# Optimization experiments

Hardware: AMD Instinct MI355X
Metric: run time of the kernel (lower is better)

Reference implementation:

```python
import jax, jax.numpy as jnp
import numpy as np

# Static dims (see shape_source)
B, S, D = 4, 4096, 1024      # batch, seq, d_model
H, E, K = 4096, 8, 2         # ffn hidden, num experts, top_k
GS = 128                     # group size = sqrt(B*S)
G = (B * S) // GS            # 128 groups, zero padding
CAP = 32                     # expert capacity after clamping


def setup_inputs() -> dict:
    key = jax.random.key(0)
    ks = jax.random.split(key, 8)
    std = jnp.float32(0.02)
    return {
        "x": jax.random.normal(ks[0], (B, S, D), jnp.float32),
        "gate_w": jax.random.normal(ks[1], (D, E), jnp.float32) * std,
        "gate_b": jnp.zeros((E,), jnp.float32),
        "keys": jax.random.normal(ks[2], (D, E, H), jnp.float32) * std,
        "key_b": jnp.zeros((E, H), jnp.float32),
        "values": jax.random.normal(ks[3], (H, E, D), jnp.float32) * std,
        "value_b": jnp.zeros((E, D), jnp.float32),
        "s_keys": jax.random.normal(ks[4], (D, 1, H), jnp.float32) * std,
        "s_key_b": jnp.zeros((1, H), jnp.float32),
        "s_values": jax.random.normal(ks[5], (H, 1, D), jnp.float32) * std,
        "s_value_b": jnp.zeros((1, D), jnp.float32),
    }


def reference(x, gate_w, gate_b, keys, key_b, values, value_b,
              s_keys, s_key_b, s_values, s_value_b):
    # ---- group tokens: [B,S,D] -> [G,GS,D] (B*S divisible by GS, no pad) ----
    xg = x.reshape(G, GS, D)

    # ---- Router (inference path: no aux loss) ----
    logits = jnp.einsum('gsd,de->gse', xg, gate_w) + gate_b          # [G,GS,E]
    probs = jax.nn.softmax(logits, axis=-1)
    gate, idx = jax.lax.top_k(probs, K)                              # [G,GS,K]
    mask = jax.nn.one_hot(idx, E, dtype=gate.dtype)                  # [G,GS,K,E]
    # position within each expert's capacity buffer (1-based where assigned)
    pos = jnp.cumsum(mask, axis=1) * mask                            # [G,GS,K,E]
    valid = (pos < CAP).astype(gate.dtype)
    pos_oh = jax.nn.one_hot(pos.astype(jnp.int32), CAP, dtype=gate.dtype)  # [G,GS,K,E,CAP]
    # combine tensor: sum over top-k, drop slot 0 (unassigned) -> [G,GS,E,CAP-1]
    combine = jnp.einsum('gsk,gske,gskec->gsec', gate, valid, pos_oh)[..., 1:]
    dispatch = (combine > 0).astype(x.dtype)                         # dispatch mask

    # ---- dispatch -> per-expert FFN -> combine ----
    exp_in = jnp.einsum('gsec,gsd->gecd', dispatch, xg)              # [G,E,CAP-1,D]
    h = jax.nn.gelu(jnp.einsum('gecd,deh->gech', exp_in, keys)
                    + key_b[None, :, None, :])                       # [G,E,CAP-1,H]
    eo = jnp.einsum('gech,hed->gecd', h, values) + value_b[None, :, None, :]
    moe = jnp.einsum('gsec,gecd->gsd', combine, eo)                  # [G,GS,D]

    # ---- shared expert (num_shared_experts == 1; mean over 1 is identity) ----
    sh = jax.nn.gelu(jnp.einsum('gsd,dh->gsh', xg, s_keys[:, 0, :]) + s_key_b[0])
    shared = jnp.einsum('gsh,hd->gsd', sh, s_values[:, 0, :]) + s_value_b[0]

    return (moe + shared).reshape(B, S, D)
```

## Files before the change

### kernel.cpp

```cpp
#include <hip/hip_runtime.h>
#include <hip/hip_bf16.h>

typedef unsigned short u16;
typedef __attribute__((ext_vector_type(8))) __bf16 bf16x8;
typedef __attribute__((ext_vector_type(4))) float f32x4;

#define TOK 16384
#define DM  1024
#define HD  4096
#define NE  8
#define NG  128
#define GSZ 128
#define CAPM 31
#define MEP (NG*32)

static __device__ __forceinline__ u16 f2b(float f) {
  union { float f; unsigned u; } v; v.f = f;
  unsigned r = v.u + 0x7fffu + ((v.u >> 16) & 1u);
  return (u16)(r >> 16);
}
static __device__ __forceinline__ float b2f(u16 u) {
  union { unsigned u; float f; } v; v.u = (unsigned)u << 16; return v.f;
}

static __device__ __forceinline__ float gelu_f(float x) {
  float y = 0.7978845608028654f * (x + 0.044715f * x * x * x);
  float t = __expf(-2.0f * fabsf(y));
  float th = (1.0f - t) / (1.0f + t);
  th = (y < 0.0f) ? -th : th;
  return 0.5f * x * (1.0f + th);
}

static __device__ __forceinline__ void gl2lds16(const void* g, void* l) {
  __builtin_amdgcn_global_load_lds(
      (const __attribute__((address_space(1))) void*)g,
      (__attribute__((address_space(3))) void*)l, 16, 0, 0);
}

__global__ __launch_bounds__(256) void k_router(
    const float* __restrict__ x, const float* __restrict__ gw,
    const float* __restrict__ gb, int* __restrict__ e_sel,
    float* __restrict__ gsel) {
  int wave = threadIdx.x >> 6, lane = threadIdx.x & 63;
  int t = blockIdx.x * 4 + wave;
  const float* xr = x + (size_t)t * DM;
  double acc[8] = {0,0,0,0,0,0,0,0};
  for (int d0 = lane * 4; d0 < DM; d0 += 256) {
    float4 xv = *(const float4*)(xr + d0);
    float xa[4] = {xv.x, xv.y, xv.z, xv.w};
    const float* g0 = gw + (size_t)d0 * NE;
#pragma unroll
    for (int dd = 0; dd < 4; ++dd)
#pragma unroll
      for (int e = 0; e < 8; ++e)
        acc[e] += (double)xa[dd] * (double)g0[dd * 8 + e];
  }
#pragma unroll
  for (int off = 32; off > 0; off >>= 1)
#pragma unroll
    for (int e = 0; e < 8; ++e)
      acc[e] += __shfl_down(acc[e], off, 64);
  if (lane == 0) {
    float l[8];
#pragma unroll
    for (int e = 0; e < 8; ++e) l[e] = (float)acc[e] + gb[e];
    int e0 = 0;
    for (int e = 1; e < 8; ++e) if (l[e] > l[e0]) e0 = e;
    int e1 = (e0 == 0) ? 1 : 0;
    for (int e = 0; e < 8; ++e) if (e != e0 && l[e] > l[e1]) e1 = e;
    float m = l[e0], s = 0.f, p[8];
    for (int e = 0; e < 8; ++e) { p[e] = expf(l[e] - m); s += p[e]; }
    e_sel[t] = e0; e_sel[TOK + t] = e1;
    gsel[t] = p[e0] / s; gsel[TOK + t] = p[e1] / s;
  }
}

__global__ void k_assign(const int* __restrict__ e_sel,
                         int* __restrict__ tok_slot, int* __restrict__ slot_tok) {
  int g = blockIdx.x;
  for (int i = threadIdx.x; i < NE * 32 * 2; i += 64) {
    int e = i >> 6, rem = i & 63, c = rem >> 1, k = rem & 1;
    slot_tok[((size_t)(e * MEP + g * 32 + c)) * 2 + k] = -1;
  }
  __syncthreads();
  if (threadIdx.x == 0) {
    int cnt[2][NE];
    for (int k = 0; k < 2; ++k) for (int e = 0; e < NE; ++e) cnt[k][e] = 0;
    for (int s = 0; s < GSZ; ++s) {
      int t = g * GSZ + s;
      for (int k = 0; k < 2; ++k) {
        int e = e_sel[k * TOK + t];
        int r = ++cnt[k][e];
        if (r <= CAPM) {
          int m = e * MEP + g * 32 + (r - 1);
          tok_slot[k * TOK + t] = m;
          slot_tok[(size_t)m * 2 + k] = t;
        } else tok_slot[k * TOK + t] = -1;
      }
    }
  }
}

__global__ __launch_bounds__(128) void k_build_expin(
    const float* __restrict__ x, const int* __restrict__ slot_tok,
    u16* __restrict__ exp_in) {
  int m = blockIdx.x;
  int t0 = slot_tok[(size_t)m * 2], t1 = slot_tok[(size_t)m * 2 + 1];
  int d = threadIdx.x * 8;
  float v[8] = {0,0,0,0,0,0,0,0};
  if (t0 >= 0) {
    const float4* p = (const float4*)(x + (size_t)t0 * DM + d);
    float4 a = p[0], b = p[1];
    v[0]+=a.x; v[1]+=a.y; v[2]+=a.z; v[3]+=a.w;
    v[4]+=b.x; v[5]+=b.y; v[6]+=b.z; v[7]+=b.w;
  }
  if (t1 >= 0) {
    const float4* p = (const float4*)(x + (size_t)t1 * DM + d);
    float4 a = p[0], b = p[1];
    v[0]+=a.x; v[1]+=a.y; v[2]+=a.z; v[3]+=a.w;
    v[4]+=b.x; v[5]+=b.y; v[6]+=b.z; v[7]+=b.w;
  }
  ushort4 o0, o1;
  o0.x=f2b(v[0]); o0.y=f2b(v[1]); o0.z=f2b(v[2]); o0.w=f2b(v[3]);
  o1.x=f2b(v[4]); o1.y=f2b(v[5]); o1.z=f2b(v[6]); o1.w=f2b(v[7]);
  *(ushort4*)(exp_in + (size_t)m * DM + d) = o0;
  *(ushort4*)(exp_in + (size_t)m * DM + d + 4) = o1;
}

__global__ __launch_bounds__(256) void k_cast_bf16(
    const float* __restrict__ in, u16* __restrict__ out, size_t n) {
  size_t i = ((size_t)blockIdx.x * 256 + threadIdx.x) * 4;
  if (i >= n) return;
  float4 v = *(const float4*)(in + i);
  ushort4 o; o.x=f2b(v.x); o.y=f2b(v.y); o.z=f2b(v.z); o.w=f2b(v.w);
  *(ushort4*)(out + i) = o;
}

__global__ __launch_bounds__(256) void k_transpose(
    const float* __restrict__ in, u16* __restrict__ out,
    int K, int N, int rs) {
  __shared__ float tile[32][33];
  int k0 = blockIdx.x * 32, n0 = blockIdx.y * 32;
  int tx = threadIdx.x & 31, ty = threadIdx.x >> 5;
#pragma unroll
  for (int i = 0; i < 4; ++i)
    tile[ty + i * 8][tx] = in[(size_t)(k0 + ty + i * 8) * rs + n0 + tx];
  __syncthreads();
#pragma unroll
  for (int i = 0; i < 4; ++i) {
    int n = ty + i * 8;
    out[(size_t)(n0 + n) * K + k0 + tx] = f2b(tile[tx][n]);
  }
}


#define PH_MID() \
  __builtin_amdgcn_s_setprio(1);

#define PH_END() \
  __builtin_amdgcn_s_setprio(0); \
  asm volatile("s_waitcnt vmcnt(4)" ::: "memory"); \
  __builtin_amdgcn_s_barrier();

#define PH_END0() \
  __builtin_amdgcn_s_setprio(0); \
  asm volatile("s_waitcnt vmcnt(0)" ::: "memory"); \
  __builtin_amdgcn_s_barrier();

#define PH_ENDN() \
  __builtin_amdgcn_s_setprio(0); \
  __builtin_amdgcn_s_barrier();

#define STG(gp, ld, lds) \
  gl2lds16((gp) + (size_t)srow * (ld) + scol, (lds) + sdst); \
  gl2lds16((gp) + (size_t)(srow + 64) * (ld) + scol, (lds) + 4096 + sdst);

#define RD_A(SLOT) \
  _Pragma("unroll") for (int k2 = 0; k2 < 2; ++k2) \
    _Pragma("unroll") for (int mi = 0; mi < 4; ++mi) \
      a[k2][mi] = *(const bf16x8*)(&HA[SLOT][0] + offA[k2][mi]);

#define RD_BA(SLOT) \
  _Pragma("unroll") for (int k2 = 0; k2 < 2; ++k2) \
    _Pragma("unroll") for (int ni = 0; ni < 2; ++ni) \
      bA[k2][ni] = *(const bf16x8*)(&HB[SLOT][0] + offB[k2][ni]);

#define RD_BB(SLOT) \
  _Pragma("unroll") for (int k2 = 0; k2 < 2; ++k2) \
    _Pragma("unroll") for (int ni = 0; ni < 2; ++ni) \
      bB[k2][ni] = *(const bf16x8*)(&HB[SLOT][0] + offB[k2][ni]);

#define MM(BM, MOFF, NOFF) \
  _Pragma("unroll") for (int k2 = 0; k2 < 2; ++k2) \
    _Pragma("unroll") for (int mi = 0; mi < 4; ++mi) \
      _Pragma("unroll") for (int ni = 0; ni < 2; ++ni) \
        acc[mi + MOFF][ni + NOFF] = __builtin_amdgcn_mfma_f32_16x16x32_bf16( \
            a[k2][mi], BM[k2][ni], acc[mi + MOFF][ni + NOFF], 0, 0, 0);

#define TILE(T, SA0, SA1, SB0, SB1, DA0, DA1, DB0, DB1) { \
  const u16* An = Ab + ((T) + 1) * 64; \
  const u16* Bn = Bb + ((T) + 1) * 64; \
  RD_A(SA0); RD_BA(SB0); \
  STG(An, lda, &HA[DA0][0]); \
  PH_MID(); MM(bA, 0, 0); PH_END(); \
  RD_BB(SB1); \
  STG(Bn, ldb, &HB[DB0][0]); \
  PH_MID(); MM(bB, 0, 2); PH_END(); \
  RD_A(SA1); \
  STG(Bn + (size_t)128 * ldb, ldb, &HB[DB1][0]); \
  PH_MID(); MM(bB, 4, 2); PH_END(); \
  STG(An + (size_t)128 * lda, lda, &HA[DA1][0]); \
  PH_MID(); MM(bA, 4, 0); PH_END(); \
}

#define TILE_LAST(SA0, SA1, SB0, SB1) { \
  RD_A(SA0); RD_BA(SB0); \
  PH_MID(); MM(bA, 0, 0); PH_END0(); \
  RD_BB(SB1); \
  PH_MID(); MM(bB, 0, 2); PH_ENDN(); \
  RD_A(SA1); \
  PH_MID(); MM(bB, 4, 2); PH_ENDN(); \
  PH_MID(); MM(bA, 4, 0); PH_ENDN(); \
}

template <int EPI>
__global__ __launch_bounds__(512, 2) void k_gemm8p(
    const u16* __restrict__ A, size_t sAe, int lda,
    const u16* __restrict__ B, size_t sBe, int ldb,
    void* __restrict__ Cv, size_t sCe, int ldc,
    const float* __restrict__ bias, int sBiasE, int K, int gx, int gy) {
  __shared__ __align__(16) u16 HA[4][128 * 64];
  __shared__ __align__(16) u16 HB[4][128 * 64];
  const int tid = threadIdx.x;
  const int lane = tid & 63, wid = tid >> 6;
  const int wr = wid >> 2, wc = wid & 3;
  const int la15 = lane & 15, hi = lane >> 4;

  int nwg = gridDim.x, per = nwg >> 3;
  int wg = (blockIdx.x & 7) * per + (blockIdx.x >> 3);
  int bx = wg % gx, tmp = wg / gx;
  int by = tmp % gy, z = tmp / gy;

  const u16* Ab = A + (size_t)z * sAe + (size_t)(bx * 256) * lda;
  const u16* Bb = B + (size_t)z * sBe + (size_t)(by * 256) * ldb;

  int offA[2][4], offB[2][2];
#pragma unroll
  for (int k2 = 0; k2 < 2; ++k2) {
    int sl = k2 * 4 + hi;
#pragma unroll
    for (int mi = 0; mi < 4; ++mi) {
      int r = (mi * 2 + wr) * 16 + la15;
      offA[k2][mi] = r * 64 + ((sl ^ (r & 7)) << 3);
    }
#pragma unroll
    for (int ni = 0; ni < 2; ++ni) {
      int r = (ni * 4 + wc) * 16 + la15;
      offB[k2][ni] = r * 64 + ((sl ^ (r & 7)) << 3);
    }
  }
  const int srow = tid >> 3;
  const int scol = (((tid & 7) ^ (srow & 7)) << 3);
  const int sdst = (tid & ~63) * 8;

  f32x4 acc[8][4] = {};
  const int NT = K >> 6;

  bf16x8 a[2][4], bA[2][2], bB[2][2];

  STG(Ab, lda, &HA[0][0]);
  STG(Bb, ldb, &HB[0][0]);
  STG(Bb + (size_t)128 * ldb, ldb, &HB[1][0]);
  STG(Ab + (size_t)128 * lda, lda, &HA[1][0]);
  asm volatile("s_waitcnt vmcnt(0)" ::: "memory");
  __builtin_amdgcn_s_barrier();

  for (int t = 0; t + 2 < NT; t += 2) {
    TILE(t,     0, 1, 0, 1, 2, 3, 2, 3);
    TILE(t + 1, 2, 3, 2, 3, 0, 1, 0, 1);
  }
  TILE(NT - 2, 0, 1, 0, 1, 2, 3, 2, 3);
  TILE_LAST(2, 3, 2, 3);

  const int hi4 = hi << 2;
#pragma unroll
  for (int ni = 0; ni < 4; ++ni) {
    int col = by * 256 + (ni * 4 + wc) * 16 + la15;
    float bv = bias[(size_t)z * sBiasE + col];
#pragma unroll
    for (int mi = 0; mi < 8; ++mi) {
      int row0 = bx * 256 + (mi * 2 + wr) * 16 + hi4;
      f32x4 v = acc[mi][ni];
#pragma unroll
      for (int j = 0; j < 4; ++j) {
        int row = row0 + j;
        float val = v[j] + bv;
        if (EPI == 0)
          ((u16*)Cv)[(size_t)z * sCe + (size_t)row * ldc + col] = f2b(gelu_f(val));
        else if (EPI == 1)
          ((u16*)Cv)[(size_t)z * sCe + (size_t)row * ldc + col] = f2b(val);
        else
          ((float*)Cv)[(size_t)z * sCe + (size_t)row * ldc + col] = val;
      }
    }
  }
}

__global__ __launch_bounds__(256) void k_combine(
    const int* __restrict__ tok_slot, const float* __restrict__ gsel,
    const u16* __restrict__ eo, float* __restrict__ out) {
  int t = blockIdx.x;
  int d = threadIdx.x * 4;
  float4 v = *(float4*)(out + (size_t)t * DM + d);
#pragma unroll
  for (int k = 0; k < 2; ++k) {
    int m = tok_slot[k * TOK + t];
    if (m >= 0) {
      float g = gsel[k * TOK + t];
      ushort4 e = *(const ushort4*)(eo + (size_t)m * DM + d);
      v.x += g * b2f(e.x); v.y += g * b2f(e.y);
      v.z += g * b2f(e.z); v.w += g * b2f(e.w);
    }
  }
  *(float4*)(out + (size_t)t * DM + d) = v;
}

__global__ void k_report(float* out, float code) { out[0] = code; }

extern "C" void kernel_launch(void* const* d_in, const int* in_sizes, int n_in,
                              void* d_out, int out_size, void* d_ws, size_t ws_size,
                              hipStream_t stream) {
  (void)in_sizes; (void)n_in;
  const float* x     = (const float*)d_in[0];
  const float* gw    = (const float*)d_in[1];
  const float* gb    = (const float*)d_in[2];
  const float* keys  = (const float*)d_in[3];
  const float* keyb  = (const float*)d_in[4];
  const float* vals  = (const float*)d_in[5];
  const float* valb  = (const float*)d_in[6];
  const float* skey  = (const float*)d_in[7];
  const float* skeyb = (const float*)d_in[8];
  const float* sval  = (const float*)d_in[9];
  const float* svalb = (const float*)d_in[10];
  float* out = (float*)d_out;

  char* ws = (char*)d_ws;
  size_t off = 0;
  auto alloc = [&](size_t bytes) -> char* {
    char* p = ws + off; off += (bytes + 255) & ~(size_t)255; return p;
  };
  int*   e_sel    = (int*)  alloc(2 * TOK * 4);
  float* gsel     = (float*)alloc(2 * TOK * 4);
  int*   tok_slot = (int*)  alloc(2 * TOK * 4);
  int*   slot_tok = (int*)  alloc((size_t)NE * MEP * 2 * 4);

  size_t off_r1 = off;
  u16* xb     = (u16*)alloc((size_t)TOK * DM * 2);
  u16* skT    = (u16*)alloc((size_t)HD * DM * 2);
  u16* svT    = (u16*)alloc((size_t)DM * HD * 2);
  u16* exp_in = (u16*)alloc((size_t)NE * MEP * DM * 2);
  u16* eo = (u16*)(ws + off_r1);
  size_t eo_end = off_r1 + (size_t)NE * MEP * DM * 2;
  if (eo_end > off) off = eo_end;

  u16* keysT = (u16*)alloc((size_t)NE * HD * DM * 2);
  u16* valsT = (u16*)alloc((size_t)NE * DM * HD * 2);

  size_t sh_b = (size_t)TOK * HD * 2;
  size_t h_b  = (size_t)NE * MEP * HD * 2;
  u16* sh = (u16*)(ws + off);
  u16* h  = (u16*)(ws + off);
  size_t need = off + (sh_b > h_b ? sh_b : h_b);

  if (need > ws_size) {
    hipMemsetAsync(d_out, 0, (size_t)out_size * 4, stream);
    k_report<<<1, 1, 0, stream>>>(out, -(float)(ws_size >> 20));
    return;
  }

  k_router<<<TOK / 4, 256, 0, stream>>>(x, gw, gb, e_sel, gsel);
  k_assign<<<NG, 64, 0, stream>>>(e_sel, tok_slot, slot_tok);
  k_build_expin<<<NE * MEP, 128, 0, stream>>>(x, slot_tok, exp_in);

  k_cast_bf16<<<(TOK * DM / 4) / 256, 256, 0, stream>>>(x, xb, (size_t)TOK * DM);
  k_transpose<<<dim3(DM / 32, HD / 32), 256, 0, stream>>>(skey, skT, DM, HD, HD);
  k_transpose<<<dim3(HD / 32, DM / 32), 256, 0, stream>>>(sval, svT, HD, DM, DM);
  for (int e = 0; e < NE; ++e) {
    k_transpose<<<dim3(DM / 32, HD / 32), 256, 0, stream>>>(
        keys + (size_t)e * HD, keysT + (size_t)e * HD * DM, DM, HD, NE * HD);
    k_transpose<<<dim3(HD / 32, DM / 32), 256, 0, stream>>>(
        vals + (size_t)e * DM, valsT + (size_t)e * DM * HD, HD, DM, NE * DM);
  }

  k_gemm8p<0><<<(TOK/256)*(HD/256), 512, 0, stream>>>(
      xb, 0, DM, skT, 0, DM, sh, 0, HD, skeyb, 0, DM, TOK/256, HD/256);
  k_gemm8p<2><<<(TOK/256)*(DM/256), 512, 0, stream>>>(
      sh, 0, HD, svT, 0, HD, out, 0, DM, svalb, 0, HD, TOK/256, DM/256);

  k_gemm8p<0><<<(MEP/256)*(HD/256)*NE, 512, 0, stream>>>(
      exp_in, (size_t)MEP * DM, DM, keysT, (size_t)HD * DM, DM,
      h, (size_t)MEP * HD, HD, keyb, HD, DM, MEP/256, HD/256);
  k_gemm8p<1><<<(MEP/256)*(DM/256)*NE, 512, 0, stream>>>(
      h, (size_t)MEP * HD, HD, valsT, (size_t)DM * HD, HD,
      eo, (size_t)MEP * DM, DM, valb, DM, HD, MEP/256, DM/256);

  k_combine<<<TOK, 256, 0, stream>>>(tok_slot, gsel, eo, out);
}
```

Before: 1.224 ms.

## Fuse bf16 cast into router, combine into shared GEMM epilogue, batch transposes

The router kernel now also writes the bf16 copy of x, which removes the separate cast kernel, and expert input building reads that bf16 copy. Per-expert weight transposes become single launches using blockIdx.z. The MoE combine step moves into the epilogue of the shared expert's second GEMM, which is reordered to run last, so the fp32 output is not re-read and re-written. The fused epilogue does scattered 2-byte gathers from the expert outputs, which may be poorly coalesced, and expert inputs are now summed from bf16-rounded values.

```diff
diff --git a/kernel.cpp b/kernel.cpp
--- a/kernel.cpp
+++ b/kernel.cpp
@@ -40,13 +40,15 @@
 __global__ __launch_bounds__(256) void k_router(
     const float* __restrict__ x, const float* __restrict__ gw,
     const float* __restrict__ gb, int* __restrict__ e_sel,
-    float* __restrict__ gsel) {
+    float* __restrict__ gsel, u16* __restrict__ xb) {
   int wave = threadIdx.x >> 6, lane = threadIdx.x & 63;
   int t = blockIdx.x * 4 + wave;
   const float* xr = x + (size_t)t * DM;
   double acc[8] = {0,0,0,0,0,0,0,0};
   for (int d0 = lane * 4; d0 < DM; d0 += 256) {
     float4 xv = *(const float4*)(xr + d0);
+    ushort4 xo; xo.x=f2b(xv.x); xo.y=f2b(xv.y); xo.z=f2b(xv.z); xo.w=f2b(xv.w);
+    *(ushort4*)(xb + (size_t)t * DM + d0) = xo;
     float xa[4] = {xv.x, xv.y, xv.z, xv.w};
     const float* g0 = gw + (size_t)d0 * NE;
 #pragma unroll
@@ -102,23 +104,23 @@
 }
 
 __global__ __launch_bounds__(128) void k_build_expin(
-    const float* __restrict__ x, const int* __restrict__ slot_tok,
+    const u16* __restrict__ xb, const int* __restrict__ slot_tok,
     u16* __restrict__ exp_in) {
   int m = blockIdx.x;
   int t0 = slot_tok[(size_t)m * 2], t1 = slot_tok[(size_t)m * 2 + 1];
   int d = threadIdx.x * 8;
   float v[8] = {0,0,0,0,0,0,0,0};
   if (t0 >= 0) {
-    const float4* p = (const float4*)(x + (size_t)t0 * DM + d);
-    float4 a = p[0], b = p[1];
-    v[0]+=a.x; v[1]+=a.y; v[2]+=a.z; v[3]+=a.w;
-    v[4]+=b.x; v[5]+=b.y; v[6]+=b.z; v[7]+=b.w;
+    const ushort4* p = (const ushort4*)(xb + (size_t)t0 * DM + d);
+    ushort4 a = p[0], b = p[1];
+    v[0]+=b2f(a.x); v[1]+=b2f(a.y); v[2]+=b2f(a.z); v[3]+=b2f(a.w);
+    v[4]+=b2f(b.x); v[5]+=b2f(b.y); v[6]+=b2f(b.z); v[7]+=b2f(b.w);
   }
   if (t1 >= 0) {
-    const float4* p = (const float4*)(x + (size_t)t1 * DM + d);
-    float4 a = p[0], b = p[1];
-    v[0]+=a.x; v[1]+=a.y; v[2]+=a.z; v[3]+=a.w;
-    v[4]+=b.x; v[5]+=b.y; v[6]+=b.z; v[7]+=b.w;
+    const ushort4* p = (const ushort4*)(xb + (size_t)t1 * DM + d);
+    ushort4 a = p[0], b = p[1];
+    v[0]+=b2f(a.x); v[1]+=b2f(a.y); v[2]+=b2f(a.z); v[3]+=b2f(a.w);
+    v[4]+=b2f(b.x); v[5]+=b2f(b.y); v[6]+=b2f(b.z); v[7]+=b2f(b.w);
   }
   ushort4 o0, o1;
   o0.x=f2b(v[0]); o0.y=f2b(v[1]); o0.z=f2b(v[2]); o0.w=f2b(v[3]);
@@ -127,19 +129,12 @@
   *(ushort4*)(exp_in + (size_t)m * DM + d + 4) = o1;
 }
 
-__global__ __launch_bounds__(256) void k_cast_bf16(
-    const float* __restrict__ in, u16* __restrict__ out, size_t n) {
-  size_t i = ((size_t)blockIdx.x * 256 + threadIdx.x) * 4;
-  if (i >= n) return;
-  float4 v = *(const float4*)(in + i);
-  ushort4 o; o.x=f2b(v.x); o.y=f2b(v.y); o.z=f2b(v.z); o.w=f2b(v.w);
-  *(ushort4*)(out + i) = o;
-}
-
 __global__ __launch_bounds__(256) void k_transpose(
     const float* __restrict__ in, u16* __restrict__ out,
-    int K, int N, int rs) {
+    int K, int N, int rs, size_t izo, size_t ozo) {
   __shared__ float tile[32][33];
+  in += (size_t)blockIdx.z * izo;
+  out += (size_t)blockIdx.z * ozo;
   int k0 = blockIdx.x * 32, n0 = blockIdx.y * 32;
   int tx = threadIdx.x & 31, ty = threadIdx.x >> 5;
 #pragma unroll
@@ -228,7 +223,9 @@
     const u16* __restrict__ A, size_t sAe, int lda,
     const u16* __restrict__ B, size_t sBe, int ldb,
     void* __restrict__ Cv, size_t sCe, int ldc,
-    const float* __restrict__ bias, int sBiasE, int K, int gx, int gy) {
+    const float* __restrict__ bias, int sBiasE, int K, int gx, int gy,
+    const u16* __restrict__ eo, const int* __restrict__ tsl,
+    const float* __restrict__ gs) {
   __shared__ __align__(16) u16 HA[4][128 * 64];
   __shared__ __align__(16) u16 HB[4][128 * 64];
   const int tid = threadIdx.x;
@@ -283,46 +280,51 @@
   TILE_LAST(2, 3, 2, 3);
 
   const int hi4 = hi << 2;
-#pragma unroll
-  for (int ni = 0; ni < 4; ++ni) {
-    int col = by * 256 + (ni * 4 + wc) * 16 + la15;
-    float bv = bias[(size_t)z * sBiasE + col];
+  if (EPI == 3) {
+    float bv[4];
+#pragma unroll
+    for (int ni = 0; ni < 4; ++ni)
+      bv[ni] = bias[by * 256 + (ni * 4 + wc) * 16 + la15];
 #pragma unroll
     for (int mi = 0; mi < 8; ++mi) {
-      int row0 = bx * 256 + (mi * 2 + wr) * 16 + hi4;
-      f32x4 v = acc[mi][ni];
 #pragma unroll
       for (int j = 0; j < 4; ++j) {
-        int row = row0 + j;
-        float val = v[j] + bv;
-        if (EPI == 0)
-          ((u16*)Cv)[(size_t)z * sCe + (size_t)row * ldc + col] = f2b(gelu_f(val));
-        else if (EPI == 1)
-          ((u16*)Cv)[(size_t)z * sCe + (size_t)row * ldc + col] = f2b(val);
-        else
-          ((float*)Cv)[(size_t)z * sCe + (size_t)row * ldc + col] = val;
+        int t = bx * 256 + (mi * 2 + wr) * 16 + hi4 + j;
+        int m0 = tsl[t], m1 = tsl[TOK + t];
+        float g0 = gs[t], g1 = gs[TOK + t];
+#pragma unroll
+        for (int ni = 0; ni < 4; ++ni) {
+          int col = by * 256 + (ni * 4 + wc) * 16 + la15;
+          float val = acc[mi][ni][j] + bv[ni];
+          if (m0 >= 0) val += g0 * b2f(eo[(size_t)m0 * DM + col]);
+          if (m1 >= 0) val += g1 * b2f(eo[(size_t)m1 * DM + col]);
+          ((float*)Cv)[(size_t)t * ldc + col] = val;
+        }
       }
     }
-  }
-}
-
-__global__ __launch_bounds__(256) void k_combine(
-    const int* __restrict__ tok_slot, const float* __restrict__ gsel,
-    const u16* __restrict__ eo, float* __restrict__ out) {
-  int t = blockIdx.x;
-  int d = threadIdx.x * 4;
-  float4 v = *(float4*)(out + (size_t)t * DM + d);
-#pragma unroll
-  for (int k = 0; k < 2; ++k) {
-    int m = tok_slot[k * TOK + t];
-    if (m >= 0) {
-      float g = gsel[k * TOK + t];
-      ushort4 e = *(const ushort4*)(eo + (size_t)m * DM + d);
-      v.x += g * b2f(e.x); v.y += g * b2f(e.y);
-      v.z += g * b2f(e.z); v.w += g * b2f(e.w);
+  } else {
+#pragma unroll
+    for (int ni = 0; ni < 4; ++ni) {
+      int col = by * 256 + (ni * 4 + wc) * 16 + la15;
+      float bvv = bias[(size_t)z * sBiasE + col];
+#pragma unroll
+      for (int mi = 0; mi < 8; ++mi) {
+        int row0 = bx * 256 + (mi * 2 + wr) * 16 + hi4;
+        f32x4 v = acc[mi][ni];
+#pragma unroll
+        for (int j = 0; j < 4; ++j) {
+          int row = row0 + j;
+          float val = v[j] + bvv;
+          if (EPI == 0)
+            ((u16*)Cv)[(size_t)z * sCe + (size_t)row * ldc + col] = f2b(gelu_f(val));
+          else if (EPI == 1)
+            ((u16*)Cv)[(size_t)z * sCe + (size_t)row * ldc + col] = f2b(val);
+          else
+            ((float*)Cv)[(size_t)z * sCe + (size_t)row * ldc + col] = val;
+        }
+      }
     }
   }
-  *(float4*)(out + (size_t)t * DM + d) = v;
 }
 
 __global__ void k_report(float* out, float code) { out[0] = code; }
@@ -354,17 +356,13 @@
   int*   tok_slot = (int*)  alloc(2 * TOK * 4);
   int*   slot_tok = (int*)  alloc((size_t)NE * MEP * 2 * 4);
 
-  size_t off_r1 = off;
   u16* xb     = (u16*)alloc((size_t)TOK * DM * 2);
   u16* skT    = (u16*)alloc((size_t)HD * DM * 2);
   u16* svT    = (u16*)alloc((size_t)DM * HD * 2);
   u16* exp_in = (u16*)alloc((size_t)NE * MEP * DM * 2);
-  u16* eo = (u16*)(ws + off_r1);
-  size_t eo_end = off_r1 + (size_t)NE * MEP * DM * 2;
-  if (eo_end > off) off = eo_end;
-
-  u16* keysT = (u16*)alloc((size_t)NE * HD * DM * 2);
-  u16* valsT = (u16*)alloc((size_t)NE * DM * HD * 2);
+  u16* eo     = exp_in;
+  u16* keysT  = (u16*)alloc((size_t)NE * HD * DM * 2);
+  u16* valsT  = (u16*)alloc((size_t)NE * DM * HD * 2);
 
   size_t sh_b = (size_t)TOK * HD * 2;
   size_t h_b  = (size_t)NE * MEP * HD * 2;
@@ -378,31 +376,32 @@
     return;
   }
 
-  k_router<<<TOK / 4, 256, 0, stream>>>(x, gw, gb, e_sel, gsel);
+  k_router<<<TOK / 4, 256, 0, stream>>>(x, gw, gb, e_sel, gsel, xb);
   k_assign<<<NG, 64, 0, stream>>>(e_sel, tok_slot, slot_tok);
-  k_build_expin<<<NE * MEP, 128, 0, stream>>>(x, slot_tok, exp_in);
-
-  k_cast_bf16<<<(TOK * DM / 4) / 256, 256, 0, stream>>>(x, xb, (size_t)TOK * DM);
-  k_transpose<<<dim3(DM / 32, HD / 32), 256, 0, stream>>>(skey, skT, DM, HD, HD);
-  k_transpose<<<dim3(HD / 32, DM / 32), 256, 0, stream>>>(sval, svT, HD, DM, DM);
-  for (int e = 0; e < NE; ++e) {
-    k_transpose<<<dim3(DM / 32, HD / 32), 256, 0, stream>>>(
-        keys + (size_t)e * HD, keysT + (size_t)e * HD * DM, DM, HD, NE * HD);
-    k_transpose<<<dim3(HD / 32, DM / 32), 256, 0, stream>>>(
-        vals + (size_t)e * DM, valsT + (size_t)e * DM * HD, HD, DM, NE * DM);
-  }
-
-  k_gemm8p<0><<<(TOK/256)*(HD/256), 512, 0, stream>>>(
-      xb, 0, DM, skT, 0, DM, sh, 0, HD, skeyb, 0, DM, TOK/256, HD/256);
-  k_gemm8p<2><<<(TOK/256)*(DM/256), 512, 0, stream>>>(
-      sh, 0, HD, svT, 0, HD, out, 0, DM, svalb, 0, HD, TOK/256, DM/256);
+  k_build_expin<<<NE * MEP, 128, 0, stream>>>(xb, slot_tok, exp_in);
+
+  k_transpose<<<dim3(DM / 32, HD / 32, 1), 256, 0, stream>>>(
+      skey, skT, DM, HD, HD, 0, 0);
+  k_transpose<<<dim3(HD / 32, DM / 32, 1), 256, 0, stream>>>(
+      sval, svT, HD, DM, DM, 0, 0);
+  k_transpose<<<dim3(DM / 32, HD / 32, NE), 256, 0, stream>>>(
+      keys, keysT, DM, HD, NE * HD, (size_t)HD, (size_t)HD * DM);
+  k_transpose<<<dim3(HD / 32, DM / 32, NE), 256, 0, stream>>>(
+      vals, valsT, HD, DM, NE * DM, (size_t)DM, (size_t)DM * HD);
 
   k_gemm8p<0><<<(MEP/256)*(HD/256)*NE, 512, 0, stream>>>(
       exp_in, (size_t)MEP * DM, DM, keysT, (size_t)HD * DM, DM,
-      h, (size_t)MEP * HD, HD, keyb, HD, DM, MEP/256, HD/256);
+      h, (size_t)MEP * HD, HD, keyb, HD, DM, MEP/256, HD/256,
+      nullptr, nullptr, nullptr);
   k_gemm8p<1><<<(MEP/256)*(DM/256)*NE, 512, 0, stream>>>(
       h, (size_t)MEP * HD, HD, valsT, (size_t)DM * HD, HD,
-      eo, (size_t)MEP * DM, DM, valb, DM, HD, MEP/256, DM/256);
-
-  k_combine<<<TOK, 256, 0, stream>>>(tok_slot, gsel, eo, out);
-}
+      eo, (size_t)MEP * DM, DM, valb, DM, HD, MEP/256, DM/256,
+      nullptr, nullptr, nullptr);
+
+  k_gemm8p<0><<<(TOK/256)*(HD/256), 512, 0, stream>>>(
+      xb, 0, DM, skT, 0, DM, sh, 0, HD, skeyb, 0, DM, TOK/256, HD/256,
+      nullptr, nullptr, nullptr);
+  k_gemm8p<3><<<(TOK/256)*(DM/256), 512, 0, stream>>>(
+      sh, 0, HD, svT, 0, HD, out, 0, DM, svalb, 0, HD, TOK/256, DM/256,
+      eo, tok_slot, gsel);
+}
```

Result: no change. 1.221 ms (-0.2%).
